# Optimization experiments

Measured on AMD Instinct MI355X. Metric: run time of the kernel, lower is better.

## Reference

```python
import jax, jax.numpy as jnp
import numpy as np

TEMPERATURE = 1.0
EPS = 1e-12  # matches torch F.normalize default eps


def setup_inputs() -> dict:
    key = jax.random.key(0)
    k1, k2 = jax.random.split(key)
    B, N, D = 8, 2048, 768
    final_features = jax.random.normal(k1, (B, N, D), dtype=jnp.float32)
    mid_features = jax.random.normal(k2, (B, N, D), dtype=jnp.float32)
    return {"final_features": final_features, "mid_features": mid_features}


def reference(final_features, mid_features):
    B, N, D = final_features.shape
    dtype = final_features.dtype

    mid = mid_features.astype(jnp.float32)
    # L2-normalize along feature dim (torch F.normalize: x / max(||x||, eps))
    norm = jnp.maximum(jnp.linalg.norm(mid, axis=-1, keepdims=True), EPS)
    mid_n = mid / norm

    # [B, N, N] cosine similarity
    sim = jnp.einsum("bnd,bmd->bnm", mid_n, mid_n)
    # zero out diagonal (add_self_similarity=False): sim * (1 - eye)
    eye = jnp.eye(N, dtype=sim.dtype)
    sim = sim * (1.0 - eye)[None, :, :]

    # confidence = row-wise max of (zeroed-diagonal) similarity
    confidence = jnp.max(sim, axis=-1)  # [B, N]

    # softmax over scaled similarities (diagonal entries are exactly 0, kept in softmax)
    weights = jax.nn.softmax(sim / TEMPERATURE, axis=-1)  # [B, N, N]

    refined = jnp.einsum("bnm,bmd->bnd", weights, final_features.astype(jnp.float32))

    cw = confidence[..., None].astype(dtype)  # [B, N, 1]
    calibrated = cw * refined.astype(dtype) + (1.0 - cw) * final_features
    return calibrated
```

## Files before the change

kernel.cpp:

```cpp
#include <hip/hip_runtime.h>
#include <hip/hip_bf16.h>

static constexpr int BB = 8;
static constexpr int NN = 2048;
static constexpr int DD = 768;

typedef __attribute__((ext_vector_type(8))) __bf16 bf16x8;
typedef __attribute__((ext_vector_type(4))) float f32x4;

__device__ __forceinline__ void gload_lds16(const __hip_bfloat16* g, __hip_bfloat16* l) {
  __builtin_amdgcn_global_load_lds(
      (const __attribute__((address_space(1))) void*)g,
      (__attribute__((address_space(3))) void*)l,
      16, 0, 0);
}

static constexpr int NORM_BLOCKS = (BB * NN) / 4;
static constexpr int TRANS_BLOCKS = BB * (NN / 64) * (DD / 64);
static constexpr int QK_BLOCKS = BB * 136;

__global__ void prep_kernel(const float* __restrict__ mid, __hip_bfloat16* __restrict__ Qn,
                            float* __restrict__ lsum, float* __restrict__ conf,
                            const float* __restrict__ F, __hip_bfloat16* __restrict__ Vt) {
  __shared__ __hip_bfloat16 tile[64][68];
  const int t = threadIdx.x;
  if (blockIdx.x < NORM_BLOCKS) {
    const int wave = t >> 6;
    const int lane = t & 63;
    const size_t row = (size_t)blockIdx.x * 4 + wave;
    if (lane == 0) { lsum[row] = 0.f; conf[row] = 0.f; }
    const float* src = mid + row * DD;

    float4 v[3];
    float ss = 0.f;
#pragma unroll
    for (int j = 0; j < 3; ++j) {
      v[j] = *(const float4*)(src + j * 256 + lane * 4);
      ss += v[j].x * v[j].x + v[j].y * v[j].y + v[j].z * v[j].z + v[j].w * v[j].w;
    }
#pragma unroll
    for (int o = 32; o; o >>= 1) ss += __shfl_xor(ss, o, 64);
    const float inv = 1.0f / fmaxf(sqrtf(ss), 1e-12f);

    __hip_bfloat16* dst = Qn + row * DD;
#pragma unroll
    for (int j = 0; j < 3; ++j) {
      union { ushort4 u; __hip_bfloat16 h[4]; } pk;
      pk.h[0] = __float2bfloat16(v[j].x * inv);
      pk.h[1] = __float2bfloat16(v[j].y * inv);
      pk.h[2] = __float2bfloat16(v[j].z * inv);
      pk.h[3] = __float2bfloat16(v[j].w * inv);
      *(ushort4*)(dst + j * 256 + lane * 4) = pk.u;
    }
  } else {
    const int bid = blockIdx.x - NORM_BLOCKS;
    const int bx = bid % (DD / 64);
    const int rest = bid / (DD / 64);
    const int by = rest & 31;
    const int b = rest >> 5;
    const int n0 = by * 64;
    const int d0 = bx * 64;
    const int tr = t >> 4;
    const int tc = t & 15;
#pragma unroll
    for (int i = 0; i < 4; ++i) {
      const int n = tr + i * 16;
      const float4 v = *(const float4*)(F + ((size_t)b * NN + n0 + n) * DD + d0 + tc * 4);
      union { ushort4 u; __hip_bfloat16 h[4]; } pk;
      pk.h[0] = __float2bfloat16(v.x);
      pk.h[1] = __float2bfloat16(v.y);
      pk.h[2] = __float2bfloat16(v.z);
      pk.h[3] = __float2bfloat16(v.w);
      *(ushort4*)&tile[n][tc * 4] = pk.u;
    }
    __syncthreads();
#pragma unroll
    for (int i = 0; i < 4; ++i) {
      const int dd = tr + i * 16;
      const int n4 = tc * 4;
      union { ushort4 u; __hip_bfloat16 h[4]; } pk;
#pragma unroll
      for (int j = 0; j < 4; ++j) pk.h[j] = tile[n4 + j][dd];
      *(ushort4*)(Vt + ((size_t)b * DD + d0 + dd) * NN + n0 + n4) = pk.u;
    }
  }
}

__global__ __launch_bounds__(256, 3) void gemm_qk_kernel(
    const __hip_bfloat16* __restrict__ Qn,
    __hip_bfloat16* __restrict__ P,
    float* __restrict__ lsum,
    unsigned* __restrict__ conf) {
  __shared__ __hip_bfloat16 smem[2 * 128 * 64];
  const int t = threadIdx.x;

  const int d = blockIdx.x;
  const int b = d & 7;
  int rem = d >> 3;
  int ti, tj;
  if (rem < 120) {
    ti = 0;
    while (rem >= 15 - ti) { rem -= 15 - ti; ++ti; }
    tj = ti + 1 + rem;
  } else {
    ti = tj = rem - 120;
  }
  const int rowBase = ti * 128;
  const int colBase = tj * 128;
  const bool offdiag = (ti != tj);

  const int lane = t & 63;
  const int wave = t >> 6;
  const int wRow = wave >> 1;
  const int wCol = wave & 1;
  const int quad = lane >> 4;
  const int l16 = lane & 15;

  const __hip_bfloat16* Abase = Qn + ((size_t)b * NN + rowBase) * DD;
  const __hip_bfloat16* Bbase = Qn + ((size_t)b * NN + colBase) * DD;

  int srow[4], scol[4], sc8[4];
#pragma unroll
  for (int i = 0; i < 4; ++i) {
    const int c = i * 256 + t;
    srow[i] = c >> 3;
    const int col8 = (c & 7) ^ ((c >> 3) & 7);
    scol[i] = col8 * 8;
    sc8[i] = c * 8;
  }

  f32x4 acc[4][4];
#pragma unroll
  for (int i = 0; i < 4; ++i)
#pragma unroll
    for (int j = 0; j < 4; ++j) acc[i][j] = (f32x4){0.f, 0.f, 0.f, 0.f};

  __hip_bfloat16* As = smem;
  __hip_bfloat16* Bs = smem + 128 * 64;

#pragma unroll
  for (int i = 0; i < 4; ++i) {
    gload_lds16(Abase + (size_t)srow[i] * DD + scol[i], As + sc8[i]);
    gload_lds16(Bbase + (size_t)srow[i] * DD + scol[i], Bs + sc8[i]);
  }

  constexpr int NK = DD / 64;
  for (int kk = 0; kk < NK; ++kk) {
    __syncthreads();
#pragma unroll
    for (int ks = 0; ks < 2; ++ks) {
      bf16x8 af[4], bfr[4];
#pragma unroll
      for (int i = 0; i < 4; ++i) {
        const int rA = wRow * 64 + i * 16 + l16;
        const int rB = wCol * 64 + i * 16 + l16;
        const int pA = (ks * 4 + quad) ^ (rA & 7);
        const int pB = (ks * 4 + quad) ^ (rB & 7);
        af[i]  = *(const bf16x8*)(As + rA * 64 + pA * 8);
        bfr[i] = *(const bf16x8*)(Bs + rB * 64 + pB * 8);
      }
#pragma unroll
      for (int mi = 0; mi < 4; ++mi)
#pragma unroll
        for (int ni = 0; ni < 4; ++ni)
          acc[mi][ni] = __builtin_amdgcn_mfma_f32_16x16x32_bf16(af[mi], bfr[ni], acc[mi][ni], 0, 0, 0);
    }
    if (kk + 1 < NK) {
      __syncthreads();
      const int k0 = (kk + 1) * 64;
#pragma unroll
      for (int i = 0; i < 4; ++i) {
        gload_lds16(Abase + (size_t)srow[i] * DD + (k0 + scol[i]), As + sc8[i]);
        gload_lds16(Bbase + (size_t)srow[i] * DD + (k0 + scol[i]), Bs + sc8[i]);
      }
    }
  }

  __hip_bfloat16* Pdir = P + ((size_t)b * NN + rowBase) * NN + colBase;
  __hip_bfloat16* Pmir = P + ((size_t)b * NN + colBase) * NN + rowBase;

  float csum[4] = {0.f, 0.f, 0.f, 0.f};
  float cmax[4] = {0.f, 0.f, 0.f, 0.f};

#pragma unroll
  for (int mi = 0; mi < 4; ++mi) {
    const int rbase = wRow * 64 + mi * 16 + quad * 4;
    float rs[4] = {0.f, 0.f, 0.f, 0.f};
    float rm[4] = {0.f, 0.f, 0.f, 0.f};
#pragma unroll
    for (int ni = 0; ni < 4; ++ni) {
      const int colL = wCol * 64 + ni * 16 + l16;
      const int col_g = colBase + colL;
      union { ushort4 u; __hip_bfloat16 h[4]; } pk;
#pragma unroll
      for (int r = 0; r < 4; ++r) {
        const int rowL = rbase + r;
        float s = acc[mi][ni][r];
        if (rowBase + rowL == col_g) s = 0.f;
        const float p = __expf(s);
        rm[r] = fmaxf(rm[r], s);
        rs[r] += p;
        csum[ni] += p;
        cmax[ni] = fmaxf(cmax[ni], s);
        pk.h[r] = __float2bfloat16(p);
        Pdir[(size_t)rowL * NN + colL] = pk.h[r];
      }
      if (offdiag) {
        *(ushort4*)(Pmir + (size_t)colL * NN + rbase) = pk.u;
      }
    }
#pragma unroll
    for (int r = 0; r < 4; ++r) {
      float ps = rs[r], mx = rm[r];
#pragma unroll
      for (int o = 1; o < 16; o <<= 1) {
        ps += __shfl_xor(ps, o, 64);
        mx = fmaxf(mx, __shfl_xor(mx, o, 64));
      }
      if (l16 == 0) {
        const int row_g = rowBase + rbase + r;
        atomicAdd(lsum + (size_t)b * NN + row_g, ps);
        atomicMax(conf + (size_t)b * NN + row_g, __float_as_uint(mx));
      }
    }
  }

  if (offdiag) {
#pragma unroll
    for (int ni = 0; ni < 4; ++ni) {
      float cs = csum[ni];
      float cm = cmax[ni];
      cs += __shfl_xor(cs, 16, 64); cm = fmaxf(cm, __shfl_xor(cm, 16, 64));
      cs += __shfl_xor(cs, 32, 64); cm = fmaxf(cm, __shfl_xor(cm, 32, 64));
      if (quad == 0) {
        const int col_g = colBase + wCol * 64 + ni * 16 + l16;
        atomicAdd(lsum + (size_t)b * NN + col_g, cs);
        atomicMax(conf + (size_t)b * NN + col_g, __float_as_uint(cm));
      }
    }
  }
}

__global__ __launch_bounds__(256) void gemm_pv_kernel(
    const __hip_bfloat16* __restrict__ P,
    const __hip_bfloat16* __restrict__ Vt,
    const float* __restrict__ lsum,
    const float* __restrict__ conf,
    const float* __restrict__ F,
    float* __restrict__ Out) {
  __shared__ __hip_bfloat16 smem[2 * (128 * 64 + 192 * 64)];

  const int d = blockIdx.x;
  const int work = (d & 7) * 64 + (d >> 3);
  const int b = work >> 6;
  const int w6 = work & 63;
  const int colBase = (w6 & 3) * 192;
  const int rowBase = (w6 >> 2) * 128;

  const int t = threadIdx.x;
  const int lane = t & 63;
  const int wave = t >> 6;
  const int wRow = wave >> 1;
  const int wCol = wave & 1;
  const int quad = lane >> 4;
  const int l16 = lane & 15;

  const __hip_bfloat16* Abase = P + (size_t)b * NN * NN + (size_t)rowBase * NN;
  const __hip_bfloat16* Bbase = Vt + (size_t)b * DD * NN + (size_t)colBase * NN;

  int srowA[4], scolA[4], sc8A[4];
#pragma unroll
  for (int i = 0; i < 4; ++i) {
    const int c = i * 256 + t;
    srowA[i] = c >> 3;
    scolA[i] = ((c & 7) ^ ((c >> 3) & 7)) * 8;
    sc8A[i] = c * 8;
  }
  int srowB[6], scolB[6], sc8B[6];
#pragma unroll
  for (int i = 0; i < 6; ++i) {
    const int c = i * 256 + t;
    srowB[i] = c >> 3;
    scolB[i] = ((c & 7) ^ ((c >> 3) & 7)) * 8;
    sc8B[i] = c * 8;
  }

  f32x4 acc[4][6];
#pragma unroll
  for (int i = 0; i < 4; ++i)
#pragma unroll
    for (int j = 0; j < 6; ++j) acc[i][j] = (f32x4){0.f, 0.f, 0.f, 0.f};

  constexpr int ABUF = 128 * 64;
  constexpr int BUFSTRIDE = 128 * 64 + 192 * 64;

  {
    __hip_bfloat16* As = smem;
    __hip_bfloat16* Bs = smem + ABUF;
#pragma unroll
    for (int i = 0; i < 4; ++i)
      gload_lds16(Abase + (size_t)srowA[i] * NN + scolA[i], As + sc8A[i]);
#pragma unroll
    for (int i = 0; i < 6; ++i)
      gload_lds16(Bbase + (size_t)srowB[i] * NN + scolB[i], Bs + sc8B[i]);
  }

  constexpr int NK = NN / 64;
  for (int kk = 0; kk < NK; ++kk) {
    const int cur = kk & 1;
    __syncthreads();
    if (kk + 1 < NK) {
      __hip_bfloat16* As = smem + (1 - cur) * BUFSTRIDE;
      __hip_bfloat16* Bs = As + ABUF;
      const int k0 = (kk + 1) * 64;
#pragma unroll
      for (int i = 0; i < 4; ++i)
        gload_lds16(Abase + (size_t)srowA[i] * NN + (k0 + scolA[i]), As + sc8A[i]);
#pragma unroll
      for (int i = 0; i < 6; ++i)
        gload_lds16(Bbase + (size_t)srowB[i] * NN + (k0 + scolB[i]), Bs + sc8B[i]);
    }
    const __hip_bfloat16* As = smem + cur * BUFSTRIDE;
    const __hip_bfloat16* Bs = As + ABUF;
#pragma unroll
    for (int ks = 0; ks < 2; ++ks) {
      bf16x8 af[4], bfr[6];
#pragma unroll
      for (int i = 0; i < 4; ++i) {
        const int rA = wRow * 64 + i * 16 + l16;
        const int pA = (ks * 4 + quad) ^ (rA & 7);
        af[i] = *(const bf16x8*)(As + rA * 64 + pA * 8);
      }
#pragma unroll
      for (int i = 0; i < 6; ++i) {
        const int rB = wCol * 96 + i * 16 + l16;
        const int pB = (ks * 4 + quad) ^ (rB & 7);
        bfr[i] = *(const bf16x8*)(Bs + rB * 64 + pB * 8);
      }
#pragma unroll
      for (int mi = 0; mi < 4; ++mi)
#pragma unroll
        for (int ni = 0; ni < 6; ++ni)
          acc[mi][ni] = __builtin_amdgcn_mfma_f32_16x16x32_bf16(af[mi], bfr[ni], acc[mi][ni], 0, 0, 0);
    }
  }

#pragma unroll
  for (int mi = 0; mi < 4; ++mi) {
#pragma unroll
    for (int r = 0; r < 4; ++r) {
      const int row_g = rowBase + wRow * 64 + mi * 16 + quad * 4 + r;
      const float li = lsum[(size_t)b * NN + row_g];
      const float cw = conf[(size_t)b * NN + row_g];
      const float inv = 1.0f / li;
      const float* frow = F + ((size_t)b * NN + row_g) * DD;
      float* orow = Out + ((size_t)b * NN + row_g) * DD;
#pragma unroll
      for (int ni = 0; ni < 6; ++ni) {
        const int col_g = colBase + wCol * 96 + ni * 16 + l16;
        const float o = acc[mi][ni][r] * inv;
        orow[col_g] = cw * o + (1.f - cw) * frow[col_g];
      }
    }
  }
}

extern "C" void kernel_launch(void* const* d_in, const int* in_sizes, int n_in,
                              void* d_out, int out_size, void* d_ws, size_t ws_size,
                              hipStream_t stream) {
  const float* F = (const float*)d_in[0];
  const float* M = (const float*)d_in[1];
  float* Out = (float*)d_out;

  char* ws = (char*)d_ws;
  __hip_bfloat16* Qn = (__hip_bfloat16*)(ws);
  __hip_bfloat16* Vt = (__hip_bfloat16*)(ws + 25165824);
  __hip_bfloat16* P  = (__hip_bfloat16*)(ws + 50331648);
  float* lsum        = (float*)(ws + 117440512);
  float* conf        = (float*)(ws + 117506048);

  prep_kernel<<<NORM_BLOCKS + TRANS_BLOCKS, 256, 0, stream>>>(M, Qn, lsum, conf, F, Vt);
  gemm_qk_kernel<<<QK_BLOCKS, 256, 0, stream>>>(Qn, P, lsum, (unsigned*)conf);
  gemm_pv_kernel<<<512, 256, 0, stream>>>(P, Vt, lsum, conf, F, Out);
}
```

Measured before the change: 251.1 us.

## Restructure PV GEMM into 256x192 tiles with 8 waves and staged barrier pipeline

The PV GEMM now runs 512-thread blocks that each compute a 256x192 output tile, halving the grid to 256 blocks. The K loop is split into four quadrant phases with explicit barriers, partial vmcnt waits and s_setprio, so the next tile's global-to-LDS loads are issued in stages interleaved with MFMA work. The aim is more data reuse per block and better overlap of memory with compute. In exchange it needs larger LDS (about 112KB), fewer blocks than CUs can hold, and carries the risk of fragile hand-counted waitcnt logic.

```diff
diff --git a/kernel.cpp b/kernel.cpp
--- a/kernel.cpp
+++ b/kernel.cpp
@@ -241,21 +241,23 @@
   }
 }
 
-__global__ __launch_bounds__(256) void gemm_pv_kernel(
+__global__ __launch_bounds__(512, 2) void gemm_pv_kernel(
     const __hip_bfloat16* __restrict__ P,
     const __hip_bfloat16* __restrict__ Vt,
     const float* __restrict__ lsum,
     const float* __restrict__ conf,
     const float* __restrict__ F,
     float* __restrict__ Out) {
-  __shared__ __hip_bfloat16 smem[2 * (128 * 64 + 192 * 64)];
-
-  const int d = blockIdx.x;
-  const int work = (d & 7) * 64 + (d >> 3);
-  const int b = work >> 6;
-  const int w6 = work & 63;
-  const int colBase = (w6 & 3) * 192;
-  const int rowBase = (w6 >> 2) * 128;
+  constexpr int ASZ = 256 * 64;
+  constexpr int BSZ = 192 * 64;
+  constexpr int BUF = ASZ + BSZ;
+  __shared__ __hip_bfloat16 smem[2 * BUF];
+
+  const int x = blockIdx.x;
+  const int b = x & 7;
+  const int work = x >> 3;
+  const int rowBase = (work >> 2) * 256;
+  const int colBase = (work & 3) * 192;
 
   const int t = threadIdx.x;
   const int lane = t & 63;
@@ -268,21 +270,19 @@
   const __hip_bfloat16* Abase = P + (size_t)b * NN * NN + (size_t)rowBase * NN;
   const __hip_bfloat16* Bbase = Vt + (size_t)b * DD * NN + (size_t)colBase * NN;
 
-  int srowA[4], scolA[4], sc8A[4];
+  int offA[4], dstA[4];
 #pragma unroll
   for (int i = 0; i < 4; ++i) {
-    const int c = i * 256 + t;
-    srowA[i] = c >> 3;
-    scolA[i] = ((c & 7) ^ ((c >> 3) & 7)) * 8;
-    sc8A[i] = c * 8;
-  }
-  int srowB[6], scolB[6], sc8B[6];
-#pragma unroll
-  for (int i = 0; i < 6; ++i) {
-    const int c = i * 256 + t;
-    srowB[i] = c >> 3;
-    scolB[i] = ((c & 7) ^ ((c >> 3) & 7)) * 8;
-    sc8B[i] = c * 8;
+    const int c = i * 512 + t;
+    offA[i] = (c >> 3) * NN + (((c & 7) ^ ((c >> 3) & 7)) << 3);
+    dstA[i] = c * 8;
+  }
+  int offB[3], dstB[3];
+#pragma unroll
+  for (int i = 0; i < 3; ++i) {
+    const int c = i * 512 + t;
+    offB[i] = (c >> 3) * NN + (((c & 7) ^ ((c >> 3) & 7)) << 3);
+    dstB[i] = c * 8;
   }
 
   f32x4 acc[4][6];
@@ -291,74 +291,143 @@
 #pragma unroll
     for (int j = 0; j < 6; ++j) acc[i][j] = (f32x4){0.f, 0.f, 0.f, 0.f};
 
-  constexpr int ABUF = 128 * 64;
-  constexpr int BUFSTRIDE = 128 * 64 + 192 * 64;
+  int rowL[4], colL[6];
+#pragma unroll
+  for (int i = 0; i < 4; ++i) rowL[i] = (i < 2) ? (wRow * 32 + i * 16) : (128 + wRow * 32 + (i - 2) * 16);
+#pragma unroll
+  for (int j = 0; j < 6; ++j) colL[j] = (j < 3) ? (wCol * 48 + j * 16) : (96 + wCol * 48 + (j - 3) * 16);
 
   {
     __hip_bfloat16* As = smem;
-    __hip_bfloat16* Bs = smem + ABUF;
-#pragma unroll
-    for (int i = 0; i < 4; ++i)
-      gload_lds16(Abase + (size_t)srowA[i] * NN + scolA[i], As + sc8A[i]);
-#pragma unroll
-    for (int i = 0; i < 6; ++i)
-      gload_lds16(Bbase + (size_t)srowB[i] * NN + scolB[i], Bs + sc8B[i]);
+    __hip_bfloat16* Bs = smem + ASZ;
+    gload_lds16(Abase + offA[0], As + dstA[0]);
+    gload_lds16(Abase + offA[1], As + dstA[1]);
+    gload_lds16(Bbase + offB[0], Bs + dstB[0]);
+    gload_lds16(Bbase + offB[1], Bs + dstB[1]);
+    gload_lds16(Bbase + offB[2], Bs + dstB[2]);
+    gload_lds16(Abase + offA[2], As + dstA[2]);
+    gload_lds16(Abase + offA[3], As + dstA[3]);
   }
 
   constexpr int NK = NN / 64;
   for (int kk = 0; kk < NK; ++kk) {
     const int cur = kk & 1;
-    __syncthreads();
-    if (kk + 1 < NK) {
-      __hip_bfloat16* As = smem + (1 - cur) * BUFSTRIDE;
-      __hip_bfloat16* Bs = As + ABUF;
-      const int k0 = (kk + 1) * 64;
-#pragma unroll
-      for (int i = 0; i < 4; ++i)
-        gload_lds16(Abase + (size_t)srowA[i] * NN + (k0 + scolA[i]), As + sc8A[i]);
-#pragma unroll
-      for (int i = 0; i < 6; ++i)
-        gload_lds16(Bbase + (size_t)srowB[i] * NN + (k0 + scolB[i]), Bs + sc8B[i]);
-    }
-    const __hip_bfloat16* As = smem + cur * BUFSTRIDE;
-    const __hip_bfloat16* Bs = As + ABUF;
-#pragma unroll
-    for (int ks = 0; ks < 2; ++ks) {
-      bf16x8 af[4], bfr[6];
-#pragma unroll
-      for (int i = 0; i < 4; ++i) {
-        const int rA = wRow * 64 + i * 16 + l16;
-        const int pA = (ks * 4 + quad) ^ (rA & 7);
-        af[i] = *(const bf16x8*)(As + rA * 64 + pA * 8);
-      }
-#pragma unroll
-      for (int i = 0; i < 6; ++i) {
-        const int rB = wCol * 96 + i * 16 + l16;
-        const int pB = (ks * 4 + quad) ^ (rB & 7);
-        bfr[i] = *(const bf16x8*)(Bs + rB * 64 + pB * 8);
-      }
-#pragma unroll
-      for (int mi = 0; mi < 4; ++mi)
-#pragma unroll
-        for (int ni = 0; ni < 6; ++ni)
-          acc[mi][ni] = __builtin_amdgcn_mfma_f32_16x16x32_bf16(af[mi], bfr[ni], acc[mi][ni], 0, 0, 0);
-    }
-  }
-
-#pragma unroll
-  for (int mi = 0; mi < 4; ++mi) {
+    const __hip_bfloat16* As = smem + cur * BUF;
+    const __hip_bfloat16* Bs = As + ASZ;
+    __hip_bfloat16* An = smem + (1 - cur) * BUF;
+    __hip_bfloat16* Bn = An + ASZ;
+    const int k0 = (kk + 1) * 64;
+    const bool more = (kk + 1 < NK);
+
+    bf16x8 af[4][2], bfr[6][2];
+
+    asm volatile("s_waitcnt vmcnt(2)" ::: "memory");
+    __builtin_amdgcn_s_barrier();
+    asm volatile("" ::: "memory");
+    if (more) {
+      gload_lds16(Abase + offA[0] + k0, An + dstA[0]);
+      gload_lds16(Abase + offA[1] + k0, An + dstA[1]);
+    }
+#pragma unroll
+    for (int i = 0; i < 2; ++i)
+#pragma unroll
+      for (int ks = 0; ks < 2; ++ks) {
+        const int r = rowL[i] + l16;
+        af[i][ks] = *(const bf16x8*)(As + r * 64 + (((ks * 4 + quad) ^ (r & 7)) << 3));
+      }
+#pragma unroll
+    for (int j = 0; j < 3; ++j)
+#pragma unroll
+      for (int ks = 0; ks < 2; ++ks) {
+        const int r = colL[j] + l16;
+        bfr[j][ks] = *(const bf16x8*)(Bs + r * 64 + (((ks * 4 + quad) ^ (r & 7)) << 3));
+      }
+    __builtin_amdgcn_s_setprio(1);
+#pragma unroll
+    for (int i = 0; i < 2; ++i)
+#pragma unroll
+      for (int j = 0; j < 3; ++j)
+#pragma unroll
+        for (int ks = 0; ks < 2; ++ks)
+          acc[i][j] = __builtin_amdgcn_mfma_f32_16x16x32_bf16(af[i][ks], bfr[j][ks], acc[i][j], 0, 0, 0);
+    __builtin_amdgcn_s_setprio(0);
+
+    __builtin_amdgcn_s_barrier();
+    asm volatile("" ::: "memory");
+    if (more) {
+      gload_lds16(Bbase + offB[0] + k0, Bn + dstB[0]);
+      gload_lds16(Bbase + offB[1] + k0, Bn + dstB[1]);
+      gload_lds16(Bbase + offB[2] + k0, Bn + dstB[2]);
+    }
+#pragma unroll
+    for (int j = 3; j < 6; ++j)
+#pragma unroll
+      for (int ks = 0; ks < 2; ++ks) {
+        const int r = colL[j] + l16;
+        bfr[j][ks] = *(const bf16x8*)(Bs + r * 64 + (((ks * 4 + quad) ^ (r & 7)) << 3));
+      }
+    __builtin_amdgcn_s_setprio(1);
+#pragma unroll
+    for (int i = 0; i < 2; ++i)
+#pragma unroll
+      for (int j = 3; j < 6; ++j)
+#pragma unroll
+        for (int ks = 0; ks < 2; ++ks)
+          acc[i][j] = __builtin_amdgcn_mfma_f32_16x16x32_bf16(af[i][ks], bfr[j][ks], acc[i][j], 0, 0, 0);
+    __builtin_amdgcn_s_setprio(0);
+
+    if (more) asm volatile("s_waitcnt vmcnt(5)" ::: "memory");
+    else      asm volatile("s_waitcnt vmcnt(0)" ::: "memory");
+    __builtin_amdgcn_s_barrier();
+    asm volatile("" ::: "memory");
+    if (more) {
+      gload_lds16(Abase + offA[2] + k0, An + dstA[2]);
+      gload_lds16(Abase + offA[3] + k0, An + dstA[3]);
+    }
+#pragma unroll
+    for (int i = 2; i < 4; ++i)
+#pragma unroll
+      for (int ks = 0; ks < 2; ++ks) {
+        const int r = rowL[i] + l16;
+        af[i][ks] = *(const bf16x8*)(As + r * 64 + (((ks * 4 + quad) ^ (r & 7)) << 3));
+      }
+    __builtin_amdgcn_s_setprio(1);
+#pragma unroll
+    for (int i = 2; i < 4; ++i)
+#pragma unroll
+      for (int j = 0; j < 3; ++j)
+#pragma unroll
+        for (int ks = 0; ks < 2; ++ks)
+          acc[i][j] = __builtin_amdgcn_mfma_f32_16x16x32_bf16(af[i][ks], bfr[j][ks], acc[i][j], 0, 0, 0);
+    __builtin_amdgcn_s_setprio(0);
+
+    __builtin_amdgcn_s_barrier();
+    asm volatile("" ::: "memory");
+    __builtin_amdgcn_s_setprio(1);
+#pragma unroll
+    for (int i = 2; i < 4; ++i)
+#pragma unroll
+      for (int j = 3; j < 6; ++j)
+#pragma unroll
+        for (int ks = 0; ks < 2; ++ks)
+          acc[i][j] = __builtin_amdgcn_mfma_f32_16x16x32_bf16(af[i][ks], bfr[j][ks], acc[i][j], 0, 0, 0);
+    __builtin_amdgcn_s_setprio(0);
+  }
+
+#pragma unroll
+  for (int i = 0; i < 4; ++i) {
 #pragma unroll
     for (int r = 0; r < 4; ++r) {
-      const int row_g = rowBase + wRow * 64 + mi * 16 + quad * 4 + r;
+      const int row_g = rowBase + rowL[i] + quad * 4 + r;
       const float li = lsum[(size_t)b * NN + row_g];
       const float cw = conf[(size_t)b * NN + row_g];
       const float inv = 1.0f / li;
       const float* frow = F + ((size_t)b * NN + row_g) * DD;
       float* orow = Out + ((size_t)b * NN + row_g) * DD;
 #pragma unroll
-      for (int ni = 0; ni < 6; ++ni) {
-        const int col_g = colBase + wCol * 96 + ni * 16 + l16;
-        const float o = acc[mi][ni][r] * inv;
+      for (int j = 0; j < 6; ++j) {
+        const int col_g = colBase + colL[j] + l16;
+        const float o = acc[i][j][r] * inv;
         orow[col_g] = cw * o + (1.f - cw) * frow[col_g];
       }
     }
@@ -381,5 +450,5 @@
 
   prep_kernel<<<NORM_BLOCKS + TRANS_BLOCKS, 256, 0, stream>>>(M, Qn, lsum, conf, F, Vt);
   gemm_qk_kernel<<<QK_BLOCKS, 256, 0, stream>>>(Qn, P, lsum, (unsigned*)conf);
-  gemm_pv_kernel<<<512, 256, 0, stream>>>(P, Vt, lsum, conf, F, Out);
+  gemm_pv_kernel<<<256, 512, 0, stream>>>(P, Vt, lsum, conf, F, Out);
 }
```

New measurement: 250.6 us. About the same (-0.2%).

## Restructure PV GEMM: 256x192 tiles, 512 threads, A fragments loaded directly from global

Applied to the files above, without the earlier changes.

The PV GEMM now uses 512-thread blocks covering 256x192 output tiles, giving 256 blocks instead of 512. The P operand is no longer staged through LDS: each wave loads its A fragments straight from global memory into registers, double-buffered across k-steps. Only Vt goes through LDS. Manual vmcnt waits, raw barriers and s_setprio are meant to overlap loads with MFMA and cut LDS traffic. The risks are uncoalesced direct global reads of P and fewer blocks than there are CUs.

```diff
diff --git a/kernel.cpp b/kernel.cpp
--- a/kernel.cpp
+++ b/kernel.cpp
@@ -241,21 +241,21 @@
   }
 }
 
-__global__ __launch_bounds__(256) void gemm_pv_kernel(
+__global__ __launch_bounds__(512, 2) void gemm_pv_kernel(
     const __hip_bfloat16* __restrict__ P,
     const __hip_bfloat16* __restrict__ Vt,
     const float* __restrict__ lsum,
     const float* __restrict__ conf,
     const float* __restrict__ F,
     float* __restrict__ Out) {
-  __shared__ __hip_bfloat16 smem[2 * (128 * 64 + 192 * 64)];
-
-  const int d = blockIdx.x;
-  const int work = (d & 7) * 64 + (d >> 3);
-  const int b = work >> 6;
-  const int w6 = work & 63;
-  const int colBase = (w6 & 3) * 192;
-  const int rowBase = (w6 >> 2) * 128;
+  constexpr int BSZ = 192 * 64;
+  __shared__ __hip_bfloat16 smem[2 * BSZ];
+
+  const int x = blockIdx.x;
+  const int b = x & 7;
+  const int work = x >> 3;
+  const int rowBase = (work >> 2) * 256;
+  const int colBase = (work & 3) * 192;
 
   const int t = threadIdx.x;
   const int lane = t & 63;
@@ -268,97 +268,106 @@
   const __hip_bfloat16* Abase = P + (size_t)b * NN * NN + (size_t)rowBase * NN;
   const __hip_bfloat16* Bbase = Vt + (size_t)b * DD * NN + (size_t)colBase * NN;
 
-  int srowA[4], scolA[4], sc8A[4];
+  int offB[3], dstB[3];
+#pragma unroll
+  for (int i = 0; i < 3; ++i) {
+    const int c = i * 512 + t;
+    offB[i] = (c >> 3) * NN + (((c & 7) ^ ((c >> 3) & 7)) << 3);
+    dstB[i] = c * 8;
+  }
+
+  int rowL[4], colL[6];
+#pragma unroll
+  for (int i = 0; i < 4; ++i) rowL[i] = (i < 2) ? (wRow * 32 + i * 16) : (128 + wRow * 32 + (i - 2) * 16);
+#pragma unroll
+  for (int j = 0; j < 6; ++j) colL[j] = (j < 3) ? (wCol * 48 + j * 16) : (96 + wCol * 48 + (j - 3) * 16);
+
+  const __hip_bfloat16* Arow[4];
+#pragma unroll
+  for (int i = 0; i < 4; ++i) Arow[i] = Abase + (size_t)(rowL[i] + l16) * NN + quad * 8;
+
+  f32x4 acc[4][6];
+#pragma unroll
+  for (int i = 0; i < 4; ++i)
+#pragma unroll
+    for (int j = 0; j < 6; ++j) acc[i][j] = (f32x4){0.f, 0.f, 0.f, 0.f};
+
+  constexpr int NK = NN / 64;
+  bf16x8 afA[4][2], afB[4][2];
+
+  {
+    __hip_bfloat16* Bs = smem;
+    gload_lds16(Bbase + offB[0], Bs + dstB[0]);
+    gload_lds16(Bbase + offB[1], Bs + dstB[1]);
+    gload_lds16(Bbase + offB[2], Bs + dstB[2]);
+#pragma unroll
+    for (int i = 0; i < 4; ++i)
+#pragma unroll
+      for (int ks = 0; ks < 2; ++ks)
+        afA[i][ks] = *(const bf16x8*)(Arow[i] + ks * 32);
+  }
+
+#define PV_TILE(afC, afN, CUR, KK)                                                      \
+  do {                                                                                  \
+    asm volatile("s_waitcnt vmcnt(8)" ::: "memory");     \
+    __builtin_amdgcn_s_barrier();                                                       \
+    asm volatile("" ::: "memory");                                                      \
+    if ((KK) + 1 < NK) {                                                                \
+      __hip_bfloat16* Bn = smem + (1 - (CUR)) * BSZ;                                    \
+      const int kb = ((KK) + 1) * 64;                                                   \
+      gload_lds16(Bbase + offB[0] + kb, Bn + dstB[0]);                                  \
+      gload_lds16(Bbase + offB[1] + kb, Bn + dstB[1]);                                  \
+      gload_lds16(Bbase + offB[2] + kb, Bn + dstB[2]);                                  \
+      _Pragma("unroll")                                                                 \
+      for (int i = 0; i < 4; ++i) {                                                     \
+        _Pragma("unroll")                                                               \
+        for (int ks = 0; ks < 2; ++ks)                                                  \
+          afN[i][ks] = *(const bf16x8*)(Arow[i] + kb + ks * 32);                        \
+      }                                                                                 \
+    }                                                                                   \
+    const __hip_bfloat16* Bs = smem + (CUR) * BSZ;                                      \
+    bf16x8 bfr[6][2];                                                                   \
+    _Pragma("unroll")                                                                   \
+    for (int j = 0; j < 6; ++j) {                                                       \
+      _Pragma("unroll")                                                                 \
+      for (int ks = 0; ks < 2; ++ks) {                                                  \
+        const int rb = colL[j] + l16;                                                   \
+        bfr[j][ks] = *(const bf16x8*)(Bs + rb * 64 + (((ks * 4 + quad) ^ (rb & 7)) << 3)); \
+      }                                                                                 \
+    }                                                                                   \
+    __builtin_amdgcn_s_setprio(1);                                                      \
+    _Pragma("unroll")                                                                   \
+    for (int i = 0; i < 4; ++i) {                                                       \
+      _Pragma("unroll")                                                                 \
+      for (int j = 0; j < 6; ++j) {                                                     \
+        _Pragma("unroll")                                                               \
+        for (int ks = 0; ks < 2; ++ks)                                                  \
+          acc[i][j] = __builtin_amdgcn_mfma_f32_16x16x32_bf16(afC[i][ks], bfr[j][ks], acc[i][j], 0, 0, 0); \
+      }                                                                                 \
+    }                                                                                   \
+    __builtin_amdgcn_s_setprio(0);                                                      \
+  } while (0)
+
+  for (int kp = 0; kp < NK; kp += 2) {
+    PV_TILE(afA, afB, 0, kp);
+    PV_TILE(afB, afA, 1, kp + 1);
+  }
+#undef PV_TILE
+
 #pragma unroll
   for (int i = 0; i < 4; ++i) {
-    const int c = i * 256 + t;
-    srowA[i] = c >> 3;
-    scolA[i] = ((c & 7) ^ ((c >> 3) & 7)) * 8;
-    sc8A[i] = c * 8;
-  }
-  int srowB[6], scolB[6], sc8B[6];
-#pragma unroll
-  for (int i = 0; i < 6; ++i) {
-    const int c = i * 256 + t;
-    srowB[i] = c >> 3;
-    scolB[i] = ((c & 7) ^ ((c >> 3) & 7)) * 8;
-    sc8B[i] = c * 8;
-  }
-
-  f32x4 acc[4][6];
-#pragma unroll
-  for (int i = 0; i < 4; ++i)
-#pragma unroll
-    for (int j = 0; j < 6; ++j) acc[i][j] = (f32x4){0.f, 0.f, 0.f, 0.f};
-
-  constexpr int ABUF = 128 * 64;
-  constexpr int BUFSTRIDE = 128 * 64 + 192 * 64;
-
-  {
-    __hip_bfloat16* As = smem;
-    __hip_bfloat16* Bs = smem + ABUF;
-#pragma unroll
-    for (int i = 0; i < 4; ++i)
-      gload_lds16(Abase + (size_t)srowA[i] * NN + scolA[i], As + sc8A[i]);
-#pragma unroll
-    for (int i = 0; i < 6; ++i)
-      gload_lds16(Bbase + (size_t)srowB[i] * NN + scolB[i], Bs + sc8B[i]);
-  }
-
-  constexpr int NK = NN / 64;
-  for (int kk = 0; kk < NK; ++kk) {
-    const int cur = kk & 1;
-    __syncthreads();
-    if (kk + 1 < NK) {
-      __hip_bfloat16* As = smem + (1 - cur) * BUFSTRIDE;
-      __hip_bfloat16* Bs = As + ABUF;
-      const int k0 = (kk + 1) * 64;
-#pragma unroll
-      for (int i = 0; i < 4; ++i)
-        gload_lds16(Abase + (size_t)srowA[i] * NN + (k0 + scolA[i]), As + sc8A[i]);
-#pragma unroll
-      for (int i = 0; i < 6; ++i)
-        gload_lds16(Bbase + (size_t)srowB[i] * NN + (k0 + scolB[i]), Bs + sc8B[i]);
-    }
-    const __hip_bfloat16* As = smem + cur * BUFSTRIDE;
-    const __hip_bfloat16* Bs = As + ABUF;
-#pragma unroll
-    for (int ks = 0; ks < 2; ++ks) {
-      bf16x8 af[4], bfr[6];
-#pragma unroll
-      for (int i = 0; i < 4; ++i) {
-        const int rA = wRow * 64 + i * 16 + l16;
-        const int pA = (ks * 4 + quad) ^ (rA & 7);
-        af[i] = *(const bf16x8*)(As + rA * 64 + pA * 8);
-      }
-#pragma unroll
-      for (int i = 0; i < 6; ++i) {
-        const int rB = wCol * 96 + i * 16 + l16;
-        const int pB = (ks * 4 + quad) ^ (rB & 7);
-        bfr[i] = *(const bf16x8*)(Bs + rB * 64 + pB * 8);
-      }
-#pragma unroll
-      for (int mi = 0; mi < 4; ++mi)
-#pragma unroll
-        for (int ni = 0; ni < 6; ++ni)
-          acc[mi][ni] = __builtin_amdgcn_mfma_f32_16x16x32_bf16(af[mi], bfr[ni], acc[mi][ni], 0, 0, 0);
-    }
-  }
-
-#pragma unroll
-  for (int mi = 0; mi < 4; ++mi) {
 #pragma unroll
     for (int r = 0; r < 4; ++r) {
-      const int row_g = rowBase + wRow * 64 + mi * 16 + quad * 4 + r;
+      const int row_g = rowBase + rowL[i] + quad * 4 + r;
       const float li = lsum[(size_t)b * NN + row_g];
       const float cw = conf[(size_t)b * NN + row_g];
       const float inv = 1.0f / li;
       const float* frow = F + ((size_t)b * NN + row_g) * DD;
       float* orow = Out + ((size_t)b * NN + row_g) * DD;
 #pragma unroll
-      for (int ni = 0; ni < 6; ++ni) {
-        const int col_g = colBase + wCol * 96 + ni * 16 + l16;
-        const float o = acc[mi][ni][r] * inv;
+      for (int j = 0; j < 6; ++j) {
+        const int col_g = colBase + colL[j] + l16;
+        const float o = acc[i][j][r] * inv;
         orow[col_g] = cw * o + (1.f - cw) * frow[col_g];
       }
     }
@@ -381,5 +390,5 @@
 
   prep_kernel<<<NORM_BLOCKS + TRANS_BLOCKS, 256, 0, stream>>>(M, Qn, lsum, conf, F, Vt);
   gemm_qk_kernel<<<QK_BLOCKS, 256, 0, stream>>>(Qn, P, lsum, (unsigned*)conf);
-  gemm_pv_kernel<<<512, 256, 0, stream>>>(P, Vt, lsum, conf, F, Out);
-}
+  gemm_pv_kernel<<<256, 512, 0, stream>>>(P, Vt, lsum, conf, F, Out);
+}
```

Result: slower. 285.6 us (+13.7%).
